# Optimization experiments

Hardware: AMD Instinct MI355X
Metric: run time of the kernel (lower is better)

## Reference

```python
import jax, jax.numpy as jnp
import numpy as np

B, S, D, HD, H = 4, 4096, 1024, 120, 1  # batch, seq, d_model, h_dim, heads (code only runs for h=1)
EPS = 1e-12  # F.normalize eps


def setup_inputs() -> dict:
    key = jax.random.key(0)
    k0, k1, k2, k3 = jax.random.split(key, 4)
    query = jax.random.normal(k0, (B, S, D), dtype=jnp.float32)
    key_t = jax.random.normal(k1, (B, S, D), dtype=jnp.float32)  # unused by forward, but a required arg
    # q_linear: Linear(d_model, h_dim*h) -> weight [HD, D], bias [HD]
    Wq = jax.random.normal(k2, (HD * H, D), dtype=jnp.float32) * np.float32(1.0 / np.sqrt(D))
    bq = jnp.zeros((HD * H,), dtype=jnp.float32)
    # weight_tensor: xavier_uniform on shape (h, d_k) = (1, 120)
    bound = np.float32(np.sqrt(6.0 / (H + HD * H)))
    weight_tensor = jax.random.uniform(k3, (H, HD * H), dtype=jnp.float32, minval=-bound, maxval=bound)
    return {"query": query, "key": key_t, "Wq": Wq, "bq": bq, "weight_tensor": weight_tensor}


def reference(query, key, Wq, bq, weight_tensor):
    # context = q_linear(query).view(B, -1, h_dim); with h=1 this is [B, S, HD]
    context = jnp.einsum('bsd,hd->bsh', query, Wq) + bq  # [B,S,HD]
    # context_fc = context.unsqueeze(0) * weight_tensor[h,1,1,d_k] -> [h,B,S,HD]
    ctx = context[None, :, :, :] * weight_tensor[:, None, None, :]  # [h,B,S,HD]
    # F.normalize(p=2, dim=-1): x / max(||x||, eps)
    nrm = jnp.sqrt(jnp.sum(ctx * ctx, axis=-1, keepdims=True))
    ctx_n = ctx / jnp.maximum(nrm, EPS)
    # per-head gram matrix then mean over heads -> [B,S,S]
    scores = jnp.einsum('hbsd,hbtd->hbst', ctx_n, ctx_n).mean(axis=0)
    # mask=None path; dropout is identity in eval mode
    return jax.nn.softmax(scores, axis=-1)
```

## Files before the change

### kernel.cpp

```cpp
#include <hip/hip_runtime.h>
#include <hip/hip_fp16.h>

#define BATCH   4
#define SEQ     4096
#define DMODEL  1024
#define HDIM    120
#define ROWS_TOTAL (BATCH * SEQ)
#define TPB     256

typedef float f32x4 __attribute__((ext_vector_type(4)));
typedef short s16x8 __attribute__((ext_vector_type(8)));

#define FRAG_PER_B ((size_t)TPB * 4 * 64)

static __device__ __forceinline__ unsigned short f2bf(float f) {
    unsigned u = __float_as_uint(f);
    u += 0x7FFFu + ((u >> 16) & 1u);
    return (unsigned short)(u >> 16);
}
static __device__ __forceinline__ s16x8 pack2x4(f32x4 lo, f32x4 hi) {
    s16x8 r;
#pragma unroll
    for (int i = 0; i < 4; ++i) r[i] = (short)f2bf(lo[i]);
#pragma unroll
    for (int i = 0; i < 4; ++i) r[4 + i] = (short)f2bf(hi[i]);
    return r;
}

__global__ __launch_bounds__(64)
void wq_frag_kernel(const float* __restrict__ Wq, const float* __restrict__ wt,
                    s16x8* __restrict__ WF)
{
    const int lane = threadIdx.x;
    const int l15  = lane & 15;
    const int l4   = lane >> 4;
    const int ct   = blockIdx.x >> 5;
    const int ks   = blockIdx.x & 31;
    const int col  = ct * 16 + l15;

    f32x4 lo = (f32x4){0.f,0.f,0.f,0.f}, hi = lo;
    if (col < HDIM) {
        const float w = wt[col];
        const float* src = Wq + (size_t)col * DMODEL + ks * 32 + l4 * 8;
        lo = *(const f32x4*)(src);
        hi = *(const f32x4*)(src + 4);
#pragma unroll
        for (int i = 0; i < 4; ++i) { lo[i] *= w; hi[i] *= w; }
    }
    WF[((size_t)(ct * 32 + ks)) * 64 + lane] = pack2x4(lo, hi);
}

__global__ __launch_bounds__(512)
void ctx_norm_kernel(const float* __restrict__ query,
                     const s16x8* __restrict__ WF,
                     const float* __restrict__ bq,
                     const float* __restrict__ wt,
                     s16x8* __restrict__ F)
{
    __shared__ unsigned short lA[2][32 * 72];
    __shared__ float lsq[32][4];
    __shared__ unsigned short lt[32][136];

    const int tid  = threadIdx.x;
    const int lane = tid & 63;
    const int wv   = tid >> 6;
    const int wr   = wv & 1;
    const int wc   = wv >> 1;
    const int l15  = lane & 15;
    const int l4   = lane >> 4;
    const int row0 = blockIdx.x * 32;

    const int arow = tid >> 4;
    const int achk = tid & 15;
    const float* aload = query + (size_t)(row0 + arow) * DMODEL + achk * 4;

    f32x4 acc[2];
#pragma unroll
    for (int n = 0; n < 2; ++n) acc[n] = (f32x4){0.f,0.f,0.f,0.f};

    auto stage = [&](int buf, const f32x4& v) {
        const unsigned u0 = (unsigned)f2bf(v[0]) | ((unsigned)f2bf(v[1]) << 16);
        const unsigned u1 = (unsigned)f2bf(v[2]) | ((unsigned)f2bf(v[3]) << 16);
        *(uint2*)&lA[buf][arow * 72 + achk * 4] = make_uint2(u0, u1);
    };

    f32x4 pr = *(const f32x4*)(aload);
    stage(0, pr);

    for (int slab = 0; slab < 16; ++slab) {
        __syncthreads();
        if (slab + 1 < 16) pr = *(const f32x4*)(aload + (slab + 1) * 64);
        const int buf = slab & 1;
#pragma unroll
        for (int ks2 = 0; ks2 < 2; ++ks2) {
            const int ks = slab * 2 + ks2;
            const s16x8 a = *(const s16x8*)&lA[buf][(wr * 16 + l15) * 72 + ks2 * 32 + l4 * 8];
#pragma unroll
            for (int n = 0; n < 2; ++n) {
                const s16x8 bfr = WF[((size_t)((wc * 2 + n) * 32 + ks)) * 64 + lane];
                acc[n] = __builtin_amdgcn_mfma_f32_16x16x32_bf16(a, bfr, acc[n], 0, 0, 0);
            }
        }
        if (slab + 1 < 16) stage(buf ^ 1, pr);
    }

    float sumsq[4] = {0.f,0.f,0.f,0.f};
#pragma unroll
    for (int n = 0; n < 2; ++n) {
        const int col = wc * 32 + n * 16 + l15;
        const float bqv = (col < HDIM) ? bq[col] * wt[col] : 0.f;
#pragma unroll
        for (int r = 0; r < 4; ++r) {
            const float v = acc[n][r] + bqv;
            acc[n][r] = v;
            sumsq[r] += v * v;
        }
    }
#pragma unroll
    for (int r = 0; r < 4; ++r) {
        float s = sumsq[r];
        s += __shfl_xor(s, 1);
        s += __shfl_xor(s, 2);
        s += __shfl_xor(s, 4);
        s += __shfl_xor(s, 8);
        sumsq[r] = s;
    }
    if (l15 == 0) {
#pragma unroll
        for (int r = 0; r < 4; ++r)
            lsq[wr * 16 + l4 * 4 + r][wc] = sumsq[r];
    }
    __syncthreads();
#pragma unroll
    for (int r = 0; r < 4; ++r) {
        const int lr = wr * 16 + l4 * 4 + r;
        const float s = lsq[lr][0] + lsq[lr][1] + lsq[lr][2] + lsq[lr][3];
        const float rinv = 1.f / fmaxf(sqrtf(s), 1e-12f);
#pragma unroll
        for (int n = 0; n < 2; ++n)
            lt[lr][wc * 32 + n * 16 + l15] = f2bf(acc[n][r] * rinv);
    }
    __syncthreads();
    {
        const int tl = wv >> 2;
        const int k4 = wv & 3;
        const s16x8 fr = *(const s16x8*)&lt[tl * 16 + l15][k4 * 32 + l4 * 8];
        F[((size_t)(blockIdx.x * 2 + tl) * 4 + k4) * 64 + lane] = fr;
    }
}

#define LOADT(dst, t) { const s16x8* _p = base + (size_t)(t) * 256;            \
    dst[0] = _p[0]; dst[1] = _p[64]; dst[2] = _p[128]; dst[3] = _p[192]; }

#define COMPT(src, t) { f32x4 _a = (f32x4){0.f, 0.f, 0.f, 0.f};                \
    _a = __builtin_amdgcn_mfma_f32_16x16x32_bf16(src[0], rfrag[0], _a, 0,0,0); \
    _a = __builtin_amdgcn_mfma_f32_16x16x32_bf16(src[1], rfrag[1], _a, 0,0,0); \
    _a = __builtin_amdgcn_mfma_f32_16x16x32_bf16(src[2], rfrag[2], _a, 0,0,0); \
    _a = __builtin_amdgcn_mfma_f32_16x16x32_bf16(src[3], rfrag[3], _a, 0,0,0); \
    const float _e0 = __expf(_a[0]), _e1 = __expf(_a[1]);                      \
    const float _e2 = __expf(_a[2]), _e3 = __expf(_a[3]);                      \
    rs += (_e0 + _e1) + (_e2 + _e3);                                           \
    const __half2 _h01 = __floats2half2_rn(_e0, _e1);                          \
    const __half2 _h23 = __floats2half2_rn(_e2, _e3);                          \
    unsigned _byte = (unsigned)(l15 * 8192 + cg * 512 + (t) * 32 + l4 * 8);    \
    _byte ^= (unsigned)(l15 << 4);                                             \
    *(uint2*)(lsbase + _byte) =                                                \
        make_uint2(*(const unsigned*)&_h01, *(const unsigned*)&_h23); }

__global__ __launch_bounds__(1024)
void gram_fused_kernel(const s16x8* __restrict__ F, float* __restrict__ out)
{
    __shared__ unsigned short lsE[16][4096];
    __shared__ float lsum[16][16];

    const int tid  = threadIdx.x;
    const int lane = tid & 63;
    const int cg   = tid >> 6;
    const int l15  = lane & 15;
    const int l4   = lane >> 4;
    char* lsbase = (char*)&lsE[0][0];

    const int u    = ((blockIdx.x & 7) << 7) | (blockIdx.x >> 3);
    const int b    = u >> 8;
    const int tr   = u & 255;
    const s16x8* Fb = F + (size_t)b * FRAG_PER_B;

    s16x8 rfrag[4];
#pragma unroll
    for (int ks = 0; ks < 4; ++ks) rfrag[ks] = Fb[((size_t)tr * 4 + ks) * 64 + lane];

    const s16x8* base = Fb + (size_t)(cg * 16) * 256 + lane;

    float rs = 0.f;
    s16x8 cA[4], cB[4], cC[4];
    LOADT(cA, 0)
    LOADT(cB, 1)
    LOADT(cC, 2)
#pragma unroll
    for (int i = 0; i < 6; ++i) {
        const int t = i * 3;
        { COMPT(cA, t)           if (t + 3 < 16) LOADT(cA, t + 3) }
        if (t + 1 < 16) { COMPT(cB, t + 1) if (t + 4 < 16) LOADT(cB, t + 4) }
        if (t + 2 < 16) { COMPT(cC, t + 2) if (t + 5 < 16) LOADT(cC, t + 5) }
    }

    rs += __shfl_xor(rs, 16);
    rs += __shfl_xor(rs, 32);
    if (lane < 16) lsum[lane][cg] = rs;
    __syncthreads();

    float s = 0.f;
#pragma unroll
    for (int w = 0; w < 16; ++w) s += lsum[cg][w];
    const float rv = 1.f / s;

    float* ob = out + ((size_t)b * SEQ + tr * 16 + cg) * SEQ;
    const unsigned swz = (unsigned)(cg << 4);
#pragma unroll
    for (int it = 0; it < 16; ++it) {
        const unsigned sbyte = (unsigned)(cg * 8192 + it * 512 + lane * 8) ^ swz;
        const uint2 d = *(const uint2*)(lsbase + sbyte);
        const float2 f01 = __half22float2(*(const __half2*)&d.x);
        const float2 f23 = __half22float2(*(const __half2*)&d.y);
        f32x4 pv;
        pv[0] = f01.x * rv;
        pv[1] = f01.y * rv;
        pv[2] = f23.x * rv;
        pv[3] = f23.y * rv;
        __builtin_nontemporal_store(pv, (f32x4*)(ob + it * 256 + lane * 4));
    }
}

extern "C" void kernel_launch(void* const* d_in, const int* in_sizes, int n_in,
                              void* d_out, int out_size, void* d_ws, size_t ws_size,
                              hipStream_t stream)
{
    const float* query = (const float*)d_in[0];
    const float* Wq    = (const float*)d_in[2];
    const float* bq    = (const float*)d_in[3];
    const float* wt    = (const float*)d_in[4];
    float* out = (float*)d_out;
    s16x8* F  = (s16x8*)d_ws;
    s16x8* WF = (s16x8*)((char*)d_ws + (size_t)4 * 1024 * 1024);

    wq_frag_kernel<<<dim3(256), dim3(64), 0, stream>>>(Wq, wt, WF);
    ctx_norm_kernel<<<dim3(ROWS_TOTAL / 32), dim3(512), 0, stream>>>(query, WF, bq, wt, F);
    gram_fused_kernel<<<dim3(BATCH * TPB), dim3(1024), 0, stream>>>(F, out);
}
```

Before: 101.0 us.

## Split softmax into separate rowsum pass and per-wave write kernel

Replaces the fused gram+softmax kernel, which needed a block-wide barrier before writing, with two kernels. The first computes row sums of exp(gram) and stores reciprocals. The second recomputes the gram tiles and has each wave stage its own strip in private LDS, then write normalized outputs without a block barrier. This removes the 1024-thread block sync and cuts LDS use per block to improve occupancy and overlap of compute with output stores. In exchange the gram MFMAs and exp are computed twice, and there is an extra launch.

```diff
diff --git a/kernel.cpp b/kernel.cpp
--- a/kernel.cpp
+++ b/kernel.cpp
@@ -149,36 +149,106 @@
     }
 }
 
-#define LOADT(dst, t) { const s16x8* _p = base + (size_t)(t) * 256;            \
+__global__ __launch_bounds__(512, 4)
+void rowsum_kernel(const s16x8* __restrict__ F, float* __restrict__ rinv)
+{
+    __shared__ float lsum[32][8];
+
+    const int tid  = threadIdx.x;
+    const int lane = tid & 63;
+    const int cg   = tid >> 6;
+    const int l15  = lane & 15;
+
+    const int u    = ((blockIdx.x & 7) << 6) | (blockIdx.x >> 3);
+    const int b    = u >> 7;
+    const int rg   = u & 127;
+    const s16x8* Fb = F + (size_t)b * FRAG_PER_B;
+
+    s16x8 rfA[4], rfB[4];
+#pragma unroll
+    for (int ks = 0; ks < 4; ++ks) {
+        rfA[ks] = Fb[((size_t)(rg * 2) * 4 + ks) * 64 + lane];
+        rfB[ks] = Fb[((size_t)(rg * 2 + 1) * 4 + ks) * 64 + lane];
+    }
+
+    const s16x8* base = Fb + (size_t)(cg * 32) * 256 + lane;
+    float rsA = 0.f, rsB = 0.f;
+
+    s16x8 cf0[4], cf1[4];
+    auto loadC = [&](s16x8* cf, int t) {
+        const s16x8* p = base + (size_t)t * 256;
+#pragma unroll
+        for (int ks = 0; ks < 4; ++ks) cf[ks] = p[ks * 64];
+    };
+    auto accum = [&](const s16x8* cf) {
+        f32x4 aA = (f32x4){0.f,0.f,0.f,0.f};
+        f32x4 aB = (f32x4){0.f,0.f,0.f,0.f};
+#pragma unroll
+        for (int ks = 0; ks < 4; ++ks) {
+            aA = __builtin_amdgcn_mfma_f32_16x16x32_bf16(cf[ks], rfA[ks], aA, 0, 0, 0);
+            aB = __builtin_amdgcn_mfma_f32_16x16x32_bf16(cf[ks], rfB[ks], aB, 0, 0, 0);
+        }
+#pragma unroll
+        for (int j = 0; j < 4; ++j) {
+            rsA += __expf(aA[j]);
+            rsB += __expf(aB[j]);
+        }
+    };
+
+    loadC(cf0, 0);
+    loadC(cf1, 1);
+    for (int t = 0; t < 32; t += 2) {
+        accum(cf0);
+        if (t + 2 < 32) loadC(cf0, t + 2);
+        accum(cf1);
+        if (t + 3 < 32) loadC(cf1, t + 3);
+    }
+
+    rsA += __shfl_xor(rsA, 16);
+    rsA += __shfl_xor(rsA, 32);
+    rsB += __shfl_xor(rsB, 16);
+    rsB += __shfl_xor(rsB, 32);
+    if (lane < 16) {
+        lsum[l15][cg]      = rsA;
+        lsum[16 + l15][cg] = rsB;
+    }
+    __syncthreads();
+    if (tid < 32) {
+        float s = 0.f;
+#pragma unroll
+        for (int w = 0; w < 8; ++w) s += lsum[tid][w];
+        rinv[(b * 128 + rg) * 32 + tid] = 1.f / s;
+    }
+}
+
+#define LOADW(dst, t) { const s16x8* _p = base + (size_t)(t) * 256;            \
     dst[0] = _p[0]; dst[1] = _p[64]; dst[2] = _p[128]; dst[3] = _p[192]; }
 
-#define COMPT(src, t) { f32x4 _a = (f32x4){0.f, 0.f, 0.f, 0.f};                \
+#define COMPW(src, t) { f32x4 _a = (f32x4){0.f, 0.f, 0.f, 0.f};                \
     _a = __builtin_amdgcn_mfma_f32_16x16x32_bf16(src[0], rfrag[0], _a, 0,0,0); \
     _a = __builtin_amdgcn_mfma_f32_16x16x32_bf16(src[1], rfrag[1], _a, 0,0,0); \
     _a = __builtin_amdgcn_mfma_f32_16x16x32_bf16(src[2], rfrag[2], _a, 0,0,0); \
     _a = __builtin_amdgcn_mfma_f32_16x16x32_bf16(src[3], rfrag[3], _a, 0,0,0); \
-    const float _e0 = __expf(_a[0]), _e1 = __expf(_a[1]);                      \
-    const float _e2 = __expf(_a[2]), _e3 = __expf(_a[3]);                      \
-    rs += (_e0 + _e1) + (_e2 + _e3);                                           \
-    const __half2 _h01 = __floats2half2_rn(_e0, _e1);                          \
-    const __half2 _h23 = __floats2half2_rn(_e2, _e3);                          \
-    unsigned _byte = (unsigned)(l15 * 8192 + cg * 512 + (t) * 32 + l4 * 8);    \
-    _byte ^= (unsigned)(l15 << 4);                                             \
-    *(uint2*)(lsbase + _byte) =                                                \
+    const __half2 _h01 = __floats2half2_rn(__expf(_a[0]), __expf(_a[1]));      \
+    const __half2 _h23 = __floats2half2_rn(__expf(_a[2]), __expf(_a[3]));      \
+    const unsigned _byte = ((unsigned)(l15 * 512 + (t) * 32 + l4 * 8))         \
+                           ^ (unsigned)(l15 << 4);                             \
+    *(uint2*)(myls + _byte) =                                                  \
         make_uint2(*(const unsigned*)&_h01, *(const unsigned*)&_h23); }
 
-__global__ __launch_bounds__(1024)
-void gram_fused_kernel(const s16x8* __restrict__ F, float* __restrict__ out)
-{
-    __shared__ unsigned short lsE[16][4096];
-    __shared__ float lsum[16][16];
+__global__ __launch_bounds__(512, 4)
+void write_wave_kernel(const s16x8* __restrict__ F,
+                       const float* __restrict__ rinv,
+                       float* __restrict__ out)
+{
+    __shared__ unsigned short lsw[8][4096];
 
     const int tid  = threadIdx.x;
     const int lane = tid & 63;
-    const int cg   = tid >> 6;
+    const int wv   = tid >> 6;
     const int l15  = lane & 15;
     const int l4   = lane >> 4;
-    char* lsbase = (char*)&lsE[0][0];
+    char* myls = (char*)&lsw[wv][0];
 
     const int u    = ((blockIdx.x & 7) << 7) | (blockIdx.x >> 3);
     const int b    = u >> 8;
@@ -189,45 +259,41 @@
 #pragma unroll
     for (int ks = 0; ks < 4; ++ks) rfrag[ks] = Fb[((size_t)tr * 4 + ks) * 64 + lane];
 
-    const s16x8* base = Fb + (size_t)(cg * 16) * 256 + lane;
-
-    float rs = 0.f;
-    s16x8 cA[4], cB[4], cC[4];
-    LOADT(cA, 0)
-    LOADT(cB, 1)
-    LOADT(cC, 2)
-#pragma unroll
-    for (int i = 0; i < 6; ++i) {
-        const int t = i * 3;
-        { COMPT(cA, t)           if (t + 3 < 16) LOADT(cA, t + 3) }
-        if (t + 1 < 16) { COMPT(cB, t + 1) if (t + 4 < 16) LOADT(cB, t + 4) }
-        if (t + 2 < 16) { COMPT(cC, t + 2) if (t + 5 < 16) LOADT(cC, t + 5) }
-    }
-
-    rs += __shfl_xor(rs, 16);
-    rs += __shfl_xor(rs, 32);
-    if (lane < 16) lsum[lane][cg] = rs;
-    __syncthreads();
-
-    float s = 0.f;
-#pragma unroll
-    for (int w = 0; w < 16; ++w) s += lsum[cg][w];
-    const float rv = 1.f / s;
-
-    float* ob = out + ((size_t)b * SEQ + tr * 16 + cg) * SEQ;
-    const unsigned swz = (unsigned)(cg << 4);
-#pragma unroll
-    for (int it = 0; it < 16; ++it) {
-        const unsigned sbyte = (unsigned)(cg * 8192 + it * 512 + lane * 8) ^ swz;
-        const uint2 d = *(const uint2*)(lsbase + sbyte);
-        const float2 f01 = __half22float2(*(const __half2*)&d.x);
-        const float2 f23 = __half22float2(*(const __half2*)&d.y);
-        f32x4 pv;
-        pv[0] = f01.x * rv;
-        pv[1] = f01.y * rv;
-        pv[2] = f23.x * rv;
-        pv[3] = f23.y * rv;
-        __builtin_nontemporal_store(pv, (f32x4*)(ob + it * 256 + lane * 4));
+    const float* rvp = rinv + (size_t)b * SEQ + tr * 16;
+    float* const obt = out + ((size_t)b * SEQ + tr * 16) * SEQ;
+
+#pragma unroll
+    for (int s = 0; s < 2; ++s) {
+        const int strip = wv + s * 8;
+        const s16x8* base = Fb + (size_t)(strip * 16) * 256 + lane;
+
+        s16x8 cA[4], cB[4], cC[4];
+        LOADW(cA, 0)
+        LOADW(cB, 1)
+        LOADW(cC, 2)
+#pragma unroll
+        for (int i = 0; i < 6; ++i) {
+            const int t = i * 3;
+            { COMPW(cA, t)           if (t + 3 < 16) LOADW(cA, t + 3) }
+            if (t + 1 < 16) { COMPW(cB, t + 1) if (t + 4 < 16) LOADW(cB, t + 4) }
+            if (t + 2 < 16) { COMPW(cC, t + 2) if (t + 5 < 16) LOADW(cC, t + 5) }
+        }
+
+        float* obs = obt + strip * 256;
+#pragma unroll
+        for (int r = 0; r < 16; ++r) {
+            const float rv = rvp[r];
+            const unsigned byte = ((unsigned)(r * 512 + lane * 8)) ^ (unsigned)(r << 4);
+            const uint2 d = *(const uint2*)(myls + byte);
+            const float2 f01 = __half22float2(*(const __half2*)&d.x);
+            const float2 f23 = __half22float2(*(const __half2*)&d.y);
+            f32x4 pv;
+            pv[0] = f01.x * rv;
+            pv[1] = f01.y * rv;
+            pv[2] = f23.x * rv;
+            pv[3] = f23.y * rv;
+            __builtin_nontemporal_store(pv, (f32x4*)(obs + (size_t)r * SEQ + lane * 4));
+        }
     }
 }
 
@@ -240,10 +306,12 @@
     const float* bq    = (const float*)d_in[3];
     const float* wt    = (const float*)d_in[4];
     float* out = (float*)d_out;
-    s16x8* F  = (s16x8*)d_ws;
-    s16x8* WF = (s16x8*)((char*)d_ws + (size_t)4 * 1024 * 1024);
+    s16x8* F    = (s16x8*)d_ws;
+    s16x8* WF   = (s16x8*)((char*)d_ws + (size_t)4 * 1024 * 1024);
+    float* rinv = (float*)((char*)d_ws + (size_t)4 * 1024 * 1024 + 256 * 1024);
 
     wq_frag_kernel<<<dim3(256), dim3(64), 0, stream>>>(Wq, wt, WF);
     ctx_norm_kernel<<<dim3(ROWS_TOTAL / 32), dim3(512), 0, stream>>>(query, WF, bq, wt, F);
-    gram_fused_kernel<<<dim3(BATCH * TPB), dim3(1024), 0, stream>>>(F, out);
-}
+    rowsum_kernel<<<dim3(512), dim3(512), 0, stream>>>(F, rinv);
+    write_wave_kernel<<<dim3(BATCH * TPB), dim3(512), 0, stream>>>(F, rinv, out);
+}
```

After: 111.0 us. 9.9% more time.

## Split gram kernel into producer/consumer warps with LDS ring buffer

Applied to the files above, without the earlier changes.

Replaces the gram+softmax kernel with a warp-specialized version. Eight waves compute exp'd score tiles into a 9-slot shared-memory ring, and eight other waves normalize and stream the rows to global memory, lagged by one row tile. Each block now covers 64 rows over 256 blocks instead of 16 rows over 1024 blocks. The goal is to overlap the MFMA/exp phase with the output store phase, which is likely the bandwidth bottleneck. The cost is half the waves doing compute, plus a __syncthreads every step.

```diff
diff --git a/kernel.cpp b/kernel.cpp
--- a/kernel.cpp
+++ b/kernel.cpp
@@ -149,85 +149,124 @@
     }
 }
 
-#define LOADT(dst, t) { const s16x8* _p = base + (size_t)(t) * 256;            \
-    dst[0] = _p[0]; dst[1] = _p[64]; dst[2] = _p[128]; dst[3] = _p[192]; }
-
-#define COMPT(src, t) { f32x4 _a = (f32x4){0.f, 0.f, 0.f, 0.f};                \
-    _a = __builtin_amdgcn_mfma_f32_16x16x32_bf16(src[0], rfrag[0], _a, 0,0,0); \
-    _a = __builtin_amdgcn_mfma_f32_16x16x32_bf16(src[1], rfrag[1], _a, 0,0,0); \
-    _a = __builtin_amdgcn_mfma_f32_16x16x32_bf16(src[2], rfrag[2], _a, 0,0,0); \
-    _a = __builtin_amdgcn_mfma_f32_16x16x32_bf16(src[3], rfrag[3], _a, 0,0,0); \
-    const float _e0 = __expf(_a[0]), _e1 = __expf(_a[1]);                      \
-    const float _e2 = __expf(_a[2]), _e3 = __expf(_a[3]);                      \
-    rs += (_e0 + _e1) + (_e2 + _e3);                                           \
-    const __half2 _h01 = __floats2half2_rn(_e0, _e1);                          \
-    const __half2 _h23 = __floats2half2_rn(_e2, _e3);                          \
-    unsigned _byte = (unsigned)(l15 * 8192 + cg * 512 + (t) * 32 + l4 * 8);    \
-    _byte ^= (unsigned)(l15 << 4);                                             \
-    *(uint2*)(lsbase + _byte) =                                                \
-        make_uint2(*(const unsigned*)&_h01, *(const unsigned*)&_h23); }
-
 __global__ __launch_bounds__(1024)
-void gram_fused_kernel(const s16x8* __restrict__ F, float* __restrict__ out)
-{
-    __shared__ unsigned short lsE[16][4096];
-    __shared__ float lsum[16][16];
+void gram_pc_kernel(const s16x8* __restrict__ F, float* __restrict__ out)
+{
+    __shared__ unsigned short ring[9][16][512];
+    __shared__ float lsum[2][16][8];
 
     const int tid  = threadIdx.x;
     const int lane = tid & 63;
-    const int cg   = tid >> 6;
+    const int wv   = tid >> 6;
     const int l15  = lane & 15;
     const int l4   = lane >> 4;
-    char* lsbase = (char*)&lsE[0][0];
-
-    const int u    = ((blockIdx.x & 7) << 7) | (blockIdx.x >> 3);
-    const int b    = u >> 8;
-    const int tr   = u & 255;
+
+    const int u    = ((blockIdx.x & 7) << 5) | (blockIdx.x >> 3);
+    const int b    = u >> 6;
+    const int rgb  = u & 63;
     const s16x8* Fb = F + (size_t)b * FRAG_PER_B;
 
     s16x8 rfrag[4];
-#pragma unroll
-    for (int ks = 0; ks < 4; ++ks) rfrag[ks] = Fb[((size_t)tr * 4 + ks) * 64 + lane];
-
-    const s16x8* base = Fb + (size_t)(cg * 16) * 256 + lane;
-
     float rs = 0.f;
-    s16x8 cA[4], cB[4], cC[4];
-    LOADT(cA, 0)
-    LOADT(cB, 1)
-    LOADT(cC, 2)
-#pragma unroll
-    for (int i = 0; i < 6; ++i) {
-        const int t = i * 3;
-        { COMPT(cA, t)           if (t + 3 < 16) LOADT(cA, t + 3) }
-        if (t + 1 < 16) { COMPT(cB, t + 1) if (t + 4 < 16) LOADT(cB, t + 4) }
-        if (t + 2 < 16) { COMPT(cC, t + 2) if (t + 5 < 16) LOADT(cC, t + 5) }
-    }
-
-    rs += __shfl_xor(rs, 16);
-    rs += __shfl_xor(rs, 32);
-    if (lane < 16) lsum[lane][cg] = rs;
-    __syncthreads();
-
-    float s = 0.f;
-#pragma unroll
-    for (int w = 0; w < 16; ++w) s += lsum[cg][w];
-    const float rv = 1.f / s;
-
-    float* ob = out + ((size_t)b * SEQ + tr * 16 + cg) * SEQ;
-    const unsigned swz = (unsigned)(cg << 4);
-#pragma unroll
-    for (int it = 0; it < 16; ++it) {
-        const unsigned sbyte = (unsigned)(cg * 8192 + it * 512 + lane * 8) ^ swz;
-        const uint2 d = *(const uint2*)(lsbase + sbyte);
-        const float2 f01 = __half22float2(*(const __half2*)&d.x);
-        const float2 f23 = __half22float2(*(const __half2*)&d.y);
-        f32x4 pv;
-        pv[0] = f01.x * rv;
-        pv[1] = f01.y * rv;
-        pv[2] = f23.x * rv;
-        pv[3] = f23.y * rv;
-        __builtin_nontemporal_store(pv, (f32x4*)(ob + it * 256 + lane * 4));
+    const int sw = wv - 8;
+    const int r0 = sw * 2, r1 = sw * 2 + 1;
+    float rv0 = 0.f, rv1 = 0.f;
+
+    auto loadC = [&](s16x8* cf, int gct) {
+        const s16x8* p = Fb + (size_t)gct * 256 + lane;
+#pragma unroll
+        for (int ks = 0; ks < 4; ++ks) cf[ks] = p[ks * 64];
+    };
+
+    for (int k = 0; k < 40; ++k) {
+        if (wv < 8) {
+            if (k < 32) {
+                const int t    = k >> 3;
+                const int uc   = k & 7;
+                const int slot = k % 9;
+                if (uc == 0) {
+#pragma unroll
+                    for (int ks = 0; ks < 4; ++ks)
+                        rfrag[ks] = Fb[((size_t)(rgb * 4 + t) * 4 + ks) * 64 + lane];
+                    rs = 0.f;
+                }
+                char* sb = (char*)&ring[slot][0][0];
+                const int gct0 = uc * 32 + wv * 4;
+                const unsigned swz = (unsigned)((l15 & 7) << 4);
+
+                auto comp = [&](const s16x8* cf, int i) {
+                    f32x4 a = (f32x4){0.f,0.f,0.f,0.f};
+#pragma unroll
+                    for (int ks = 0; ks < 4; ++ks)
+                        a = __builtin_amdgcn_mfma_f32_16x16x32_bf16(cf[ks], rfrag[ks], a, 0, 0, 0);
+                    const float e0 = __expf(a[0]), e1 = __expf(a[1]);
+                    const float e2 = __expf(a[2]), e3 = __expf(a[3]);
+                    rs += (e0 + e1) + (e2 + e3);
+                    const __half2 h01 = __floats2half2_rn(e0, e1);
+                    const __half2 h23 = __floats2half2_rn(e2, e3);
+                    const unsigned byte = ((unsigned)(l15 * 1024 + wv * 128 + i * 32 + l4 * 8)) ^ swz;
+                    *(uint2*)(sb + byte) = make_uint2(*(const unsigned*)&h01, *(const unsigned*)&h23);
+                };
+
+                s16x8 cf0[4], cf1[4];
+                loadC(cf0, gct0);
+                loadC(cf1, gct0 + 1);
+                comp(cf0, 0); loadC(cf0, gct0 + 2);
+                comp(cf1, 1); loadC(cf1, gct0 + 3);
+                comp(cf0, 2);
+                comp(cf1, 3);
+
+                if (uc == 7) {
+                    float tsum = rs;
+                    tsum += __shfl_xor(tsum, 16);
+                    tsum += __shfl_xor(tsum, 32);
+                    if (lane < 16) lsum[t & 1][l15][wv] = tsum;
+                }
+            }
+        } else {
+            if (k >= 8) {
+                const int km   = k - 8;
+                const int ts   = km >> 3;
+                const int uc   = km & 7;
+                const int slot = km % 9;
+                if (uc == 0) {
+                    float s0 = 0.f, s1 = 0.f;
+#pragma unroll
+                    for (int w = 0; w < 8; ++w) {
+                        s0 += lsum[ts & 1][r0][w];
+                        s1 += lsum[ts & 1][r1][w];
+                    }
+                    rv0 = 1.f / s0;
+                    rv1 = 1.f / s1;
+                }
+                const char* sb = (const char*)&ring[slot][0][0];
+                float* ob0 = out + ((size_t)b * SEQ + rgb * 64 + ts * 16 + r0) * SEQ + uc * 512;
+                float* ob1 = out + ((size_t)b * SEQ + rgb * 64 + ts * 16 + r1) * SEQ + uc * 512;
+#pragma unroll
+                for (int i = 0; i < 2; ++i) {
+                    const unsigned byA = ((unsigned)(r0 * 1024 + i * 512 + lane * 8))
+                                         ^ ((unsigned)((r0 & 7) << 4));
+                    const uint2 dA = *(const uint2*)(sb + byA);
+                    const float2 a01 = __half22float2(*(const __half2*)&dA.x);
+                    const float2 a23 = __half22float2(*(const __half2*)&dA.y);
+                    f32x4 pA;
+                    pA[0] = a01.x * rv0; pA[1] = a01.y * rv0;
+                    pA[2] = a23.x * rv0; pA[3] = a23.y * rv0;
+                    __builtin_nontemporal_store(pA, (f32x4*)(ob0 + i * 256 + lane * 4));
+
+                    const unsigned byB = ((unsigned)(r1 * 1024 + i * 512 + lane * 8))
+                                         ^ ((unsigned)((r1 & 7) << 4));
+                    const uint2 dB = *(const uint2*)(sb + byB);
+                    const float2 b01 = __half22float2(*(const __half2*)&dB.x);
+                    const float2 b23 = __half22float2(*(const __half2*)&dB.y);
+                    f32x4 pB;
+                    pB[0] = b01.x * rv1; pB[1] = b01.y * rv1;
+                    pB[2] = b23.x * rv1; pB[3] = b23.y * rv1;
+                    __builtin_nontemporal_store(pB, (f32x4*)(ob1 + i * 256 + lane * 4));
+                }
+            }
+        }
+        __syncthreads();
     }
 }
 
@@ -245,5 +284,5 @@
 
     wq_frag_kernel<<<dim3(256), dim3(64), 0, stream>>>(Wq, wt, WF);
     ctx_norm_kernel<<<dim3(ROWS_TOTAL / 32), dim3(512), 0, stream>>>(query, WF, bq, wt, F);
-    gram_fused_kernel<<<dim3(BATCH * TPB), dim3(1024), 0, stream>>>(F, out);
-}
+    gram_pc_kernel<<<dim3(256), dim3(1024), 0, stream>>>(F, out);
+}
```

Result: slower. 107.4 us (+6.4%).

## Process 64 rows per block in gram kernel with two-pass recompute

Applied to the files above, without the earlier changes.

The gram/softmax kernel now handles 64 query rows per block instead of 16, holding four row tiles of fragments in registers so each loaded column fragment is reused four times. A first pass computes only the row sums of exponentials. A second pass recomputes the MFMAs in four 1024-column chunks, stashes the fp16 exponentials in shared memory, and writes the normalized output. This cuts column-fragment reloads and fits the shared-memory stash to fewer rows, at the cost of doing the MFMA and exp work twice, using more registers, and launching fewer blocks (256 instead of 1024).

```diff
diff --git a/kernel.cpp b/kernel.cpp
--- a/kernel.cpp
+++ b/kernel.cpp
@@ -149,85 +149,132 @@
     }
 }
 
-#define LOADT(dst, t) { const s16x8* _p = base + (size_t)(t) * 256;            \
-    dst[0] = _p[0]; dst[1] = _p[64]; dst[2] = _p[128]; dst[3] = _p[192]; }
-
-#define COMPT(src, t) { f32x4 _a = (f32x4){0.f, 0.f, 0.f, 0.f};                \
-    _a = __builtin_amdgcn_mfma_f32_16x16x32_bf16(src[0], rfrag[0], _a, 0,0,0); \
-    _a = __builtin_amdgcn_mfma_f32_16x16x32_bf16(src[1], rfrag[1], _a, 0,0,0); \
-    _a = __builtin_amdgcn_mfma_f32_16x16x32_bf16(src[2], rfrag[2], _a, 0,0,0); \
-    _a = __builtin_amdgcn_mfma_f32_16x16x32_bf16(src[3], rfrag[3], _a, 0,0,0); \
-    const float _e0 = __expf(_a[0]), _e1 = __expf(_a[1]);                      \
-    const float _e2 = __expf(_a[2]), _e3 = __expf(_a[3]);                      \
-    rs += (_e0 + _e1) + (_e2 + _e3);                                           \
-    const __half2 _h01 = __floats2half2_rn(_e0, _e1);                          \
-    const __half2 _h23 = __floats2half2_rn(_e2, _e3);                          \
-    unsigned _byte = (unsigned)(l15 * 8192 + cg * 512 + (t) * 32 + l4 * 8);    \
-    _byte ^= (unsigned)(l15 << 4);                                             \
-    *(uint2*)(lsbase + _byte) =                                                \
-        make_uint2(*(const unsigned*)&_h01, *(const unsigned*)&_h23); }
-
 __global__ __launch_bounds__(1024)
-void gram_fused_kernel(const s16x8* __restrict__ F, float* __restrict__ out)
-{
-    __shared__ unsigned short lsE[16][4096];
-    __shared__ float lsum[16][16];
+void gram64_kernel(const s16x8* __restrict__ F, float* __restrict__ out)
+{
+    __shared__ unsigned short stash[64 * 1024];
+    __shared__ float lsum[64][16];
 
     const int tid  = threadIdx.x;
     const int lane = tid & 63;
-    const int cg   = tid >> 6;
+    const int wv   = tid >> 6;
     const int l15  = lane & 15;
     const int l4   = lane >> 4;
-    char* lsbase = (char*)&lsE[0][0];
-
-    const int u    = ((blockIdx.x & 7) << 7) | (blockIdx.x >> 3);
-    const int b    = u >> 8;
-    const int tr   = u & 255;
+    char* lsb = (char*)&stash[0];
+
+    const int u    = ((blockIdx.x & 7) << 5) | (blockIdx.x >> 3);
+    const int b    = u >> 6;
+    const int rg   = u & 63;
     const s16x8* Fb = F + (size_t)b * FRAG_PER_B;
 
-    s16x8 rfrag[4];
-#pragma unroll
-    for (int ks = 0; ks < 4; ++ks) rfrag[ks] = Fb[((size_t)tr * 4 + ks) * 64 + lane];
-
-    const s16x8* base = Fb + (size_t)(cg * 16) * 256 + lane;
-
-    float rs = 0.f;
-    s16x8 cA[4], cB[4], cC[4];
-    LOADT(cA, 0)
-    LOADT(cB, 1)
-    LOADT(cC, 2)
-#pragma unroll
-    for (int i = 0; i < 6; ++i) {
-        const int t = i * 3;
-        { COMPT(cA, t)           if (t + 3 < 16) LOADT(cA, t + 3) }
-        if (t + 1 < 16) { COMPT(cB, t + 1) if (t + 4 < 16) LOADT(cB, t + 4) }
-        if (t + 2 < 16) { COMPT(cC, t + 2) if (t + 5 < 16) LOADT(cC, t + 5) }
-    }
-
-    rs += __shfl_xor(rs, 16);
-    rs += __shfl_xor(rs, 32);
-    if (lane < 16) lsum[lane][cg] = rs;
+    s16x8 rfrag[4][4];
+#pragma unroll
+    for (int rt = 0; rt < 4; ++rt)
+#pragma unroll
+        for (int ks = 0; ks < 4; ++ks)
+            rfrag[rt][ks] = Fb[((size_t)(rg * 4 + rt) * 4 + ks) * 64 + lane];
+
+    float rs[4] = {0.f, 0.f, 0.f, 0.f};
+    {
+        const s16x8* base = Fb + (size_t)(wv * 16) * 256 + lane;
+        s16x8 cf0[4], cf1[4];
+        auto loadC = [&](s16x8* cf, int t) {
+            const s16x8* p = base + (size_t)t * 256;
+#pragma unroll
+            for (int ks = 0; ks < 4; ++ks) cf[ks] = p[ks * 64];
+        };
+        auto accum = [&](const s16x8* cf) {
+#pragma unroll
+            for (int rt = 0; rt < 4; ++rt) {
+                f32x4 a = (f32x4){0.f,0.f,0.f,0.f};
+#pragma unroll
+                for (int ks = 0; ks < 4; ++ks)
+                    a = __builtin_amdgcn_mfma_f32_16x16x32_bf16(cf[ks], rfrag[rt][ks], a, 0, 0, 0);
+                rs[rt] += (__expf(a[0]) + __expf(a[1])) + (__expf(a[2]) + __expf(a[3]));
+            }
+        };
+        loadC(cf0, 0);
+        loadC(cf1, 1);
+        for (int t = 0; t < 16; t += 2) {
+            accum(cf0);
+            if (t + 2 < 16) loadC(cf0, t + 2);
+            accum(cf1);
+            if (t + 3 < 16) loadC(cf1, t + 3);
+        }
+    }
+#pragma unroll
+    for (int rt = 0; rt < 4; ++rt) {
+        rs[rt] += __shfl_xor(rs[rt], 16);
+        rs[rt] += __shfl_xor(rs[rt], 32);
+    }
+    if (lane < 16) {
+#pragma unroll
+        for (int rt = 0; rt < 4; ++rt) lsum[rt * 16 + l15][wv] = rs[rt];
+    }
     __syncthreads();
-
-    float s = 0.f;
-#pragma unroll
-    for (int w = 0; w < 16; ++w) s += lsum[cg][w];
-    const float rv = 1.f / s;
-
-    float* ob = out + ((size_t)b * SEQ + tr * 16 + cg) * SEQ;
-    const unsigned swz = (unsigned)(cg << 4);
-#pragma unroll
-    for (int it = 0; it < 16; ++it) {
-        const unsigned sbyte = (unsigned)(cg * 8192 + it * 512 + lane * 8) ^ swz;
-        const uint2 d = *(const uint2*)(lsbase + sbyte);
-        const float2 f01 = __half22float2(*(const __half2*)&d.x);
-        const float2 f23 = __half22float2(*(const __half2*)&d.y);
-        f32x4 pv;
-        pv[0] = f01.x * rv;
-        pv[1] = f01.y * rv;
-        pv[2] = f23.x * rv;
-        pv[3] = f23.y * rv;
-        __builtin_nontemporal_store(pv, (f32x4*)(ob + it * 256 + lane * 4));
+    float rv[4];
+#pragma unroll
+    for (int j = 0; j < 4; ++j) {
+        const int row = wv * 4 + j;
+        float s = 0.f;
+#pragma unroll
+        for (int w = 0; w < 16; ++w) s += lsum[row][w];
+        rv[j] = 1.f / s;
+    }
+
+#pragma unroll
+    for (int c = 0; c < 4; ++c) {
+        if (c > 0) __syncthreads();
+        {
+            s16x8 cfA[4], cfB[4];
+            auto loadC = [&](s16x8* cf, int i) {
+                const s16x8* p = Fb + (size_t)(c * 64 + wv * 4 + i) * 256 + lane;
+#pragma unroll
+                for (int ks = 0; ks < 4; ++ks) cf[ks] = p[ks * 64];
+            };
+            auto comp = [&](const s16x8* cf, int i) {
+#pragma unroll
+                for (int rt = 0; rt < 4; ++rt) {
+                    f32x4 a = (f32x4){0.f,0.f,0.f,0.f};
+#pragma unroll
+                    for (int ks = 0; ks < 4; ++ks)
+                        a = __builtin_amdgcn_mfma_f32_16x16x32_bf16(cf[ks], rfrag[rt][ks], a, 0, 0, 0);
+                    const __half2 h01 = __floats2half2_rn(__expf(a[0]), __expf(a[1]));
+                    const __half2 h23 = __floats2half2_rn(__expf(a[2]), __expf(a[3]));
+                    const int row = rt * 16 + l15;
+                    const unsigned byte = ((unsigned)(row * 2048 + (wv * 4 + i) * 32 + l4 * 8))
+                                          ^ (unsigned)((row & 7) << 4);
+                    *(uint2*)(lsb + byte) = make_uint2(*(const unsigned*)&h01,
+                                                       *(const unsigned*)&h23);
+                }
+            };
+            loadC(cfA, 0);
+            loadC(cfB, 1);
+            comp(cfA, 0); loadC(cfA, 2);
+            comp(cfB, 1); loadC(cfB, 3);
+            comp(cfA, 2);
+            comp(cfB, 3);
+        }
+        __syncthreads();
+#pragma unroll
+        for (int j = 0; j < 4; ++j) {
+            const int r = wv * 4 + j;
+            float* ob = out + ((size_t)b * SEQ + rg * 64 + r) * SEQ + c * 1024;
+            const unsigned rsw = (unsigned)((r & 7) << 4);
+#pragma unroll
+            for (int it = 0; it < 4; ++it) {
+                const unsigned byte = ((unsigned)(r * 2048 + it * 512 + lane * 8)) ^ rsw;
+                const uint2 d = *(const uint2*)(lsb + byte);
+                const float2 f01 = __half22float2(*(const __half2*)&d.x);
+                const float2 f23 = __half22float2(*(const __half2*)&d.y);
+                f32x4 pv;
+                pv[0] = f01.x * rv[j];
+                pv[1] = f01.y * rv[j];
+                pv[2] = f23.x * rv[j];
+                pv[3] = f23.y * rv[j];
+                __builtin_nontemporal_store(pv, (f32x4*)(ob + it * 256 + lane * 4));
+            }
+        }
     }
 }
 
@@ -245,5 +292,5 @@
 
     wq_frag_kernel<<<dim3(256), dim3(64), 0, stream>>>(Wq, wt, WF);
     ctx_norm_kernel<<<dim3(ROWS_TOTAL / 32), dim3(512), 0, stream>>>(query, WF, bq, wt, F);
-    gram_fused_kernel<<<dim3(BATCH * TPB), dim3(1024), 0, stream>>>(F, out);
-}
+    gram64_kernel<<<dim3(256), dim3(1024), 0, stream>>>(F, out);
+}
```

Measured after the change: 152.5 us. +51.0%, slower.
